# Kernel optimization log

Hardware: AMD Instinct MI355X
Metric: run time of the kernel (lower is better)

Reference implementation:

```python
import jax, jax.numpy as jnp
import numpy as np
import math

D_MODEL = 1024
NUM_HEADS = 16
HEAD_DIM = D_MODEL // NUM_HEADS
WINDOW = 5  # positions j with i - W//2 <= j <= i + W//2 are visible


def setup_inputs() -> dict:
    key = jax.random.key(0)
    ks = jax.random.split(key, 9)
    B, S = 2, 2048
    x = jax.random.normal(ks[0], (B, S, D_MODEL), dtype=jnp.float32)
    # Xavier-uniform linear weights [out, in] (torch convention), zero biases
    lim = math.sqrt(6.0 / (D_MODEL + D_MODEL))
    def w(k):
        return jax.random.uniform(k, (D_MODEL, D_MODEL), dtype=jnp.float32, minval=-lim, maxval=lim)
    return {
        'x': x,
        'Wq': w(ks[1]), 'bq': jnp.zeros((D_MODEL,), jnp.float32),
        'Wk': w(ks[2]), 'bk': jnp.zeros((D_MODEL,), jnp.float32),
        'Wv': w(ks[3]), 'bv': jnp.zeros((D_MODEL,), jnp.float32),
        'Wo': w(ks[4]), 'bo': jnp.zeros((D_MODEL,), jnp.float32),
    }


def reference(x, Wq, bq, Wk, bk, Wv, bv, Wo, bo):
    B, S, D = x.shape
    H, hd = NUM_HEADS, HEAD_DIM
    half = WINDOW // 2

    def proj(W, b):
        # torch Linear: y = x @ W.T + b ; split heads -> [B, H, S, hd]
        return (jnp.einsum('bsd,ed->bse', x, W) + b).reshape(B, S, H, hd).transpose(0, 2, 1, 3)

    q = proj(Wq, bq)
    k = proj(Wk, bk)
    v = proj(Wv, bv)

    scores = jnp.einsum('bhqd,bhkd->bhqk', q, k) / jnp.sqrt(jnp.asarray(hd, x.dtype))
    i = jnp.arange(S)[:, None]
    j = jnp.arange(S)[None, :]
    band = (j >= i - half) & (j <= i + half)  # [S, S] local window mask
    scores = jnp.where(band, scores, jnp.asarray(-1e9, x.dtype))
    attn = jax.nn.softmax(scores, axis=-1)  # dropout is identity in eval mode
    out = jnp.einsum('bhqk,bhkd->bhqd', attn, v)
    out = out.transpose(0, 2, 1, 3).reshape(B, S, D)
    return jnp.einsum('bsd,ed->bse', out, Wo) + bo
```

## Files before the change

kernel.cpp:

```cpp
#include <hip/hip_runtime.h>
#include <hip/hip_bf16.h>

typedef __bf16 bf16_t;
typedef __bf16 bf16x4 __attribute__((ext_vector_type(4)));
typedef __bf16 bf16x8 __attribute__((ext_vector_type(8)));
typedef float f32x4 __attribute__((ext_vector_type(4)));

#define S_LEN 2048
#define DMODEL 1024
#define NHEADS 16
#define HDIM 64
#define BROWS 4096
#define QKVN 3072

__device__ __forceinline__ void async16(const void* g, void* l) {
  __builtin_amdgcn_global_load_lds(
      (const __attribute__((address_space(1))) void*)g,
      (__attribute__((address_space(3))) void*)l, 16, 0, 0);
}

__global__ __launch_bounds__(256) void cvt_all_kernel(
    const float* __restrict__ x, const float* __restrict__ Wq,
    const float* __restrict__ Wk, const float* __restrict__ Wv,
    const float* __restrict__ Wo, bf16_t* __restrict__ dst) {
  const int i = blockIdx.x * 256 + threadIdx.x;
  constexpr int XN4 = (BROWS * DMODEL) / 4;
  constexpr int WN4 = (DMODEL * DMODEL) / 4;
  const float* src;
  size_t off;
  if (i < XN4) {
    src = x;
    off = (size_t)i;
  } else {
    const int wi = i - XN4;
    const int w = wi >> 18;
    off = (size_t)(wi & (WN4 - 1));
    src = (w == 0) ? Wq : (w == 1) ? Wk : (w == 2) ? Wv : Wo;
  }
  const float4 v = *(const float4*)(src + off * 4);
  bf16x4 o;
  o[0] = (bf16_t)v.x;
  o[1] = (bf16_t)v.y;
  o[2] = (bf16_t)v.z;
  o[3] = (bf16_t)v.w;
  *(bf16x4*)(dst + (size_t)i * 4) = o;
}

#define BARR __builtin_amdgcn_s_barrier()
#define LGKM0 asm volatile("s_waitcnt lgkmcnt(0)" ::: "memory")
#define VMC10 asm volatile("s_waitcnt vmcnt(10)" ::: "memory")
#define VMC0 asm volatile("s_waitcnt vmcnt(0)" ::: "memory")

__global__ __launch_bounds__(256, 2) void gemm_qkv_kernel(
    const bf16_t* __restrict__ A, const bf16_t* __restrict__ W,
    const float* __restrict__ bq, const float* __restrict__ bk,
    const float* __restrict__ bv, bf16_t* __restrict__ C) {
  constexpr int Kd = 1024;
  __shared__ char lds[81920];
  char* ldsA = lds;
  char* ldsB = lds + 32768;

  const int m0 = blockIdx.x * 128;
  const int n0 = blockIdx.y * 192;

  const int tid = threadIdx.x;
  const int lane = tid & 63;
  const int wid = tid >> 6;
  const int wr = wid >> 1;
  const int wc = wid & 1;
  const int fr = lane & 15;
  const int l16 = lane >> 4;

  f32x4 acc[4][6] = {};
  bf16x8 aS[4][2], bB[6][2];

  auto stageA = [&](int buf, int kt) {
#pragma unroll
    for (int l = 0; l < 4; ++l) {
      const int idx = l * 256 + tid;
      const int r = idx >> 3;
      const int slot = idx & 7;
      async16((const char*)(A + (size_t)(m0 + r) * Kd + kt * 64 +
                            ((slot ^ (r & 7)) << 3)),
              ldsA + buf * 16384 + r * 128 + slot * 16);
    }
  };
  auto stageB = [&](int buf, int kt) {
#pragma unroll
    for (int l = 0; l < 6; ++l) {
      const int idx = l * 256 + tid;
      const int r = idx >> 3;
      const int slot = idx & 7;
      async16((const char*)(W + (size_t)(n0 + r) * Kd + kt * 64 +
                            ((slot ^ (r & 7)) << 3)),
              ldsB + buf * 24576 + r * 128 + slot * 16);
    }
  };

  auto rdA = [&](int buf, int row, int ks) -> bf16x8 {
    return *(const bf16x8*)(ldsA + buf * 16384 + row * 128 +
                            ((((ks << 2) + l16) ^ (row & 7)) << 4));
  };
  auto rdB = [&](int buf, int row, int ks) -> bf16x8 {
    return *(const bf16x8*)(ldsB + buf * 24576 + row * 128 +
                            ((((ks << 2) + l16) ^ (row & 7)) << 4));
  };

  stageA(0, 0);
  stageB(0, 0);
  stageA(1, 1);
  stageB(1, 1);
  VMC10;
  BARR;

#pragma unroll 1
  for (int t = 0; t < 16; ++t) {
    const int buf = t & 1;
#pragma unroll
    for (int m_ = 0; m_ < 4; ++m_)
#pragma unroll
      for (int ks_ = 0; ks_ < 2; ++ks_)
        aS[m_][ks_] = rdA(buf, wr * 64 + m_ * 16 + fr, ks_);
#pragma unroll
    for (int n_ = 0; n_ < 6; ++n_)
#pragma unroll
      for (int ks_ = 0; ks_ < 2; ++ks_)
        bB[n_][ks_] = rdB(buf, wc * 96 + n_ * 16 + fr, ks_);
    LGKM0;
    BARR;
    if (t + 2 < 16) {
      stageA(buf, t + 2);
      stageB(buf, t + 2);
    }
    __builtin_amdgcn_s_setprio(1);
#pragma unroll
    for (int m_ = 0; m_ < 4; ++m_)
#pragma unroll
      for (int n_ = 0; n_ < 6; ++n_)
#pragma unroll
        for (int ks_ = 0; ks_ < 2; ++ks_)
          acc[m_][n_] = __builtin_amdgcn_mfma_f32_16x16x32_bf16(
              aS[m_][ks_], bB[n_][ks_], acc[m_][n_], 0, 0, 0);
    __builtin_amdgcn_s_setprio(0);
    if (t < 15) {
      if (t + 2 < 16) {
        VMC10;
      } else {
        VMC0;
      }
      BARR;
    }
  }

  const int cr = l16 * 4;
#pragma unroll
  for (int nf = 0; nf < 6; ++nf) {
    const int col = n0 + wc * 96 + nf * 16 + fr;
    const int mat = col >> 10;
    const float* bp = (mat == 0) ? bq : (mat == 1) ? bk : bv;
    const float bval = bp[col & 1023];
#pragma unroll
    for (int mf = 0; mf < 4; ++mf) {
      const int row = m0 + wr * 64 + mf * 16 + cr;
#pragma unroll
      for (int r = 0; r < 4; ++r)
        C[(size_t)(row + r) * QKVN + col] = (bf16_t)(acc[mf][nf][r] + bval);
    }
  }
}

__global__ __launch_bounds__(512) void gemm_o_kernel(
    const bf16_t* __restrict__ Adat, const bf16_t* __restrict__ W,
    const float* __restrict__ bias, float* __restrict__ out) {
  constexpr int Kd = 1024, Nd = 1024, BK = 32, NT = Kd / BK;
  __shared__ bf16_t ldsA[2][128 * BK];
  __shared__ bf16_t ldsB[2][128 * BK];

  const int m0 = blockIdx.x * 128;
  const int n0 = blockIdx.y * 128;

  const int tid = threadIdx.x;
  const int lane = tid & 63;
  const int wid = tid >> 6;
  const int wr = wid >> 2;
  const int wc = wid & 3;
  const int fr = lane & 15;
  const int ko = (lane >> 4) * 8;

  f32x4 acc[4][2] = {};

  auto stage = [&](int buf, int t) {
    const int k0 = t * BK;
    const int row = tid >> 2;
    const int kb = (tid & 3) * 16;
    async16((const char*)(Adat + (size_t)(m0 + row) * Kd + k0) + kb,
            (char*)ldsA[buf] + row * 64 + kb);
    async16((const char*)(W + (size_t)(n0 + row) * Kd + k0) + kb,
            (char*)ldsB[buf] + row * 64 + kb);
  };

  auto compute = [&](int buf) {
    bf16x8 af[4], bf[2];
#pragma unroll
    for (int i = 0; i < 4; ++i)
      af[i] = *(const bf16x8*)(ldsA[buf] + (wr * 64 + i * 16 + fr) * BK + ko);
#pragma unroll
    for (int j = 0; j < 2; ++j)
      bf[j] = *(const bf16x8*)(ldsB[buf] + (wc * 32 + j * 16 + fr) * BK + ko);
#pragma unroll
    for (int i = 0; i < 4; ++i)
#pragma unroll
      for (int j = 0; j < 2; ++j)
        acc[i][j] = __builtin_amdgcn_mfma_f32_16x16x32_bf16(af[i], bf[j],
                                                            acc[i][j], 0, 0, 0);
  };

  stage(0, 0);
  __syncthreads();
#pragma unroll 1
  for (int t = 0; t < NT; ++t) {
    if (t + 1 < NT) stage((t + 1) & 1, t + 1);
    compute(t & 1);
    __syncthreads();
  }

  const int cr = (lane >> 4) * 4;
#pragma unroll
  for (int j = 0; j < 2; ++j) {
    const int col = n0 + wc * 32 + j * 16 + fr;
    const float bval = bias[col];
#pragma unroll
    for (int i = 0; i < 4; ++i) {
#pragma unroll
      for (int r = 0; r < 4; ++r) {
        const int row = m0 + wr * 64 + i * 16 + cr + r;
        out[(size_t)row * Nd + col] = acc[i][j][r] + bval;
      }
    }
  }
}

#define CHUNK 256
#define TROWS 260

__global__ __launch_bounds__(256) void attn_kernel(
    const bf16_t* __restrict__ QKV, bf16_t* __restrict__ ctx) {
  __shared__ bf16_t ldsK[TROWS * HDIM];
  __shared__ bf16_t ldsV[TROWS * HDIM];

  const int tid = threadIdx.x;
  const int blk = blockIdx.x;
  const int chunk = blk & 7;
  const int bh = blk >> 3;
  const int h = bh & (NHEADS - 1);
  const int b = bh >> 4;
  const int s0 = chunk * CHUNK;

  const bf16_t* Kb = QKV + (size_t)b * S_LEN * QKVN + DMODEL + h * HDIM;
  const bf16_t* Vb = QKV + (size_t)b * S_LEN * QKVN + 2 * DMODEL + h * HDIM;

#pragma unroll
  for (int j = 0; j < 9; ++j) {
    const int i = j * 256 + tid;
    if (i < TROWS * 8) {
      const int tr = i >> 3;
      const int slot = i & 7;
      const int c = slot ^ (tr & 7);
      int gs = s0 - 2 + tr;
      gs = (gs < 0) ? 0 : (gs >= S_LEN ? S_LEN - 1 : gs);
      async16((const char*)(Kb + (size_t)gs * QKVN) + c * 16,
              (char*)ldsK + i * 16);
      async16((const char*)(Vb + (size_t)gs * QKVN) + c * 16,
              (char*)ldsV + i * 16);
    }
  }

  const int s = s0 + tid;
  const bf16_t* Qrow = QKV + ((size_t)(b * S_LEN) + s) * QKVN + h * HDIM;
  bf16x8 q8[8];
#pragma unroll
  for (int c = 0; c < 8; ++c) q8[c] = *(const bf16x8*)(Qrow + c * 8);
  float qf[64];
#pragma unroll
  for (int c = 0; c < 8; ++c)
#pragma unroll
    for (int e = 0; e < 8; ++e) qf[c * 8 + e] = (float)q8[c][e];

  __syncthreads();

  float sc[5];
#pragma unroll
  for (int jj = 0; jj < 5; ++jj) {
    const int tr = tid + jj;
    float d = 0.f;
#pragma unroll
    for (int c = 0; c < 8; ++c) {
      const bf16x8 k8 = *(const bf16x8*)(ldsK + tr * HDIM + (c ^ (tr & 7)) * 8);
#pragma unroll
      for (int e = 0; e < 8; ++e) d += qf[c * 8 + e] * (float)k8[e];
    }
    const int j = s - 2 + jj;
    sc[jj] = (j < 0 || j >= S_LEN) ? -1e30f : d * 0.125f;
  }

  float m = sc[0];
#pragma unroll
  for (int jj = 1; jj < 5; ++jj) m = fmaxf(m, sc[jj]);
  float p[5], l = 0.f;
#pragma unroll
  for (int jj = 0; jj < 5; ++jj) {
    p[jj] = __expf(sc[jj] - m);
    l += p[jj];
  }
  const float inv = 1.0f / l;
#pragma unroll
  for (int jj = 0; jj < 5; ++jj) p[jj] *= inv;

  float o[64];
#pragma unroll
  for (int e = 0; e < 64; ++e) o[e] = 0.f;
#pragma unroll
  for (int jj = 0; jj < 5; ++jj) {
    const int tr = tid + jj;
    const float pj = p[jj];
#pragma unroll
    for (int c = 0; c < 8; ++c) {
      const bf16x8 v8 = *(const bf16x8*)(ldsV + tr * HDIM + (c ^ (tr & 7)) * 8);
#pragma unroll
      for (int e = 0; e < 8; ++e) o[c * 8 + e] += pj * (float)v8[e];
    }
  }

  bf16_t* Crow = (bf16_t*)ctx + ((size_t)(b * S_LEN) + s) * DMODEL + h * HDIM;
#pragma unroll
  for (int c = 0; c < 8; ++c) {
    bf16x8 ov;
#pragma unroll
    for (int e = 0; e < 8; ++e) ov[e] = (bf16_t)o[c * 8 + e];
    *(bf16x8*)(Crow + c * 8) = ov;
  }
}

extern "C" void kernel_launch(void* const* d_in, const int* in_sizes, int n_in,
                              void* d_out, int out_size, void* d_ws,
                              size_t ws_size, hipStream_t stream) {
  const float* x = (const float*)d_in[0];
  const float* Wq = (const float*)d_in[1];
  const float* bq = (const float*)d_in[2];
  const float* Wk = (const float*)d_in[3];
  const float* bk = (const float*)d_in[4];
  const float* Wv = (const float*)d_in[5];
  const float* bv = (const float*)d_in[6];
  const float* Wo = (const float*)d_in[7];
  const float* bo = (const float*)d_in[8];
  float* out = (float*)d_out;

  const size_t mat = (size_t)BROWS * DMODEL;
  const size_t wmat = (size_t)DMODEL * DMODEL;
  bf16_t* xb = (bf16_t*)d_ws;
  bf16_t* Wqkv = xb + mat;
  bf16_t* Wob = Wqkv + 3 * wmat;
  bf16_t* QKV = Wob + wmat;
  bf16_t* ctx = QKV + 3 * mat;

  cvt_all_kernel<<<8192, 256, 0, stream>>>(x, Wq, Wk, Wv, Wo, xb);
  gemm_qkv_kernel<<<dim3(32, 16), 256, 0, stream>>>(xb, Wqkv, bq, bk, bv,
                                                    QKV);
  attn_kernel<<<256, 256, 0, stream>>>(QKV, ctx);
  gemm_o_kernel<<<dim3(32, 8), 512, 0, stream>>>(ctx, Wob, bo, out);
}
```

Baseline: 73.39 us.

## Rewrite output projection GEMM with 64x128 tiles, BK=64, swizzled LDS and prefetching

The output projection GEMM moves from 128x128 tiles with 512 threads and BK=32 to 64x128 tiles with 128 threads, BK=64, and 512 blocks. It uses an XOR-swizzled LDS layout to avoid bank conflicts and a two-stage async prefetch with explicit vmcnt waits. MFMA sections run at raised wave priority. The aim is more blocks to fill the CUs, fewer barriers per K step, and less LDS conflict cost, at the price of more register use per wave.

After: 68.10 us, median of 2. 1.08x faster.

```diff
diff --git a/kernel.cpp b/kernel.cpp
--- a/kernel.cpp
+++ b/kernel.cpp
@@ -49,6 +49,7 @@
 #define BARR __builtin_amdgcn_s_barrier()
 #define LGKM0 asm volatile("s_waitcnt lgkmcnt(0)" ::: "memory")
 #define VMC10 asm volatile("s_waitcnt vmcnt(10)" ::: "memory")
+#define VMC12 asm volatile("s_waitcnt vmcnt(12)" ::: "memory")
 #define VMC0 asm volatile("s_waitcnt vmcnt(0)" ::: "memory")
 
 __global__ __launch_bounds__(256, 2) void gemm_qkv_kernel(
@@ -169,73 +170,115 @@
   }
 }
 
-__global__ __launch_bounds__(512) void gemm_o_kernel(
-    const bf16_t* __restrict__ Adat, const bf16_t* __restrict__ W,
+__global__ __launch_bounds__(128) void gemm_o_kernel(
+    const bf16_t* __restrict__ A, const bf16_t* __restrict__ W,
     const float* __restrict__ bias, float* __restrict__ out) {
-  constexpr int Kd = 1024, Nd = 1024, BK = 32, NT = Kd / BK;
-  __shared__ bf16_t ldsA[2][128 * BK];
-  __shared__ bf16_t ldsB[2][128 * BK];
-
-  const int m0 = blockIdx.x * 128;
+  constexpr int Kd = 1024, Nd = 1024;
+  __shared__ char lds[49152];
+  char* ldsA = lds;
+  char* ldsB = lds + 16384;
+
+  const int m0 = blockIdx.x * 64;
   const int n0 = blockIdx.y * 128;
 
   const int tid = threadIdx.x;
   const int lane = tid & 63;
   const int wid = tid >> 6;
-  const int wr = wid >> 2;
-  const int wc = wid & 3;
   const int fr = lane & 15;
-  const int ko = (lane >> 4) * 8;
-
-  f32x4 acc[4][2] = {};
-
-  auto stage = [&](int buf, int t) {
-    const int k0 = t * BK;
-    const int row = tid >> 2;
-    const int kb = (tid & 3) * 16;
-    async16((const char*)(Adat + (size_t)(m0 + row) * Kd + k0) + kb,
-            (char*)ldsA[buf] + row * 64 + kb);
-    async16((const char*)(W + (size_t)(n0 + row) * Kd + k0) + kb,
-            (char*)ldsB[buf] + row * 64 + kb);
-  };
-
-  auto compute = [&](int buf) {
-    bf16x8 af[4], bf[2];
-#pragma unroll
-    for (int i = 0; i < 4; ++i)
-      af[i] = *(const bf16x8*)(ldsA[buf] + (wr * 64 + i * 16 + fr) * BK + ko);
-#pragma unroll
-    for (int j = 0; j < 2; ++j)
-      bf[j] = *(const bf16x8*)(ldsB[buf] + (wc * 32 + j * 16 + fr) * BK + ko);
-#pragma unroll
-    for (int i = 0; i < 4; ++i)
-#pragma unroll
-      for (int j = 0; j < 2; ++j)
-        acc[i][j] = __builtin_amdgcn_mfma_f32_16x16x32_bf16(af[i], bf[j],
-                                                            acc[i][j], 0, 0, 0);
-  };
-
-  stage(0, 0);
-  __syncthreads();
+  const int l16 = lane >> 4;
+
+  f32x4 acc[4][4] = {};
+  bf16x8 aS[4][2], bB[4][2];
+
+  auto stageA = [&](int buf, int kt) {
+#pragma unroll
+    for (int l = 0; l < 4; ++l) {
+      const int idx = l * 128 + tid;
+      const int r = idx >> 3;
+      const int slot = idx & 7;
+      async16((const char*)(A + (size_t)(m0 + r) * Kd + kt * 64 +
+                            ((slot ^ (r & 7)) << 3)),
+              ldsA + buf * 8192 + r * 128 + slot * 16);
+    }
+  };
+  auto stageB = [&](int buf, int kt) {
+#pragma unroll
+    for (int l = 0; l < 8; ++l) {
+      const int idx = l * 128 + tid;
+      const int r = idx >> 3;
+      const int slot = idx & 7;
+      async16((const char*)(W + (size_t)(n0 + r) * Kd + kt * 64 +
+                            ((slot ^ (r & 7)) << 3)),
+              ldsB + buf * 16384 + r * 128 + slot * 16);
+    }
+  };
+
+  auto rdA = [&](int buf, int row, int ks) -> bf16x8 {
+    return *(const bf16x8*)(ldsA + buf * 8192 + row * 128 +
+                            ((((ks << 2) + l16) ^ (row & 7)) << 4));
+  };
+  auto rdB = [&](int buf, int row, int ks) -> bf16x8 {
+    return *(const bf16x8*)(ldsB + buf * 16384 + row * 128 +
+                            ((((ks << 2) + l16) ^ (row & 7)) << 4));
+  };
+
+  stageA(0, 0);
+  stageB(0, 0);
+  stageA(1, 1);
+  stageB(1, 1);
+  VMC12;
+  BARR;
+
 #pragma unroll 1
-  for (int t = 0; t < NT; ++t) {
-    if (t + 1 < NT) stage((t + 1) & 1, t + 1);
-    compute(t & 1);
-    __syncthreads();
-  }
-
-  const int cr = (lane >> 4) * 4;
-#pragma unroll
-  for (int j = 0; j < 2; ++j) {
-    const int col = n0 + wc * 32 + j * 16 + fr;
+  for (int t = 0; t < 16; ++t) {
+    const int buf = t & 1;
+#pragma unroll
+    for (int m_ = 0; m_ < 4; ++m_)
+#pragma unroll
+      for (int ks_ = 0; ks_ < 2; ++ks_)
+        aS[m_][ks_] = rdA(buf, m_ * 16 + fr, ks_);
+#pragma unroll
+    for (int n_ = 0; n_ < 4; ++n_)
+#pragma unroll
+      for (int ks_ = 0; ks_ < 2; ++ks_)
+        bB[n_][ks_] = rdB(buf, wid * 64 + n_ * 16 + fr, ks_);
+    LGKM0;
+    BARR;
+    if (t + 2 < 16) {
+      stageA(buf, t + 2);
+      stageB(buf, t + 2);
+    }
+    __builtin_amdgcn_s_setprio(1);
+#pragma unroll
+    for (int m_ = 0; m_ < 4; ++m_)
+#pragma unroll
+      for (int n_ = 0; n_ < 4; ++n_)
+#pragma unroll
+        for (int ks_ = 0; ks_ < 2; ++ks_)
+          acc[m_][n_] = __builtin_amdgcn_mfma_f32_16x16x32_bf16(
+              aS[m_][ks_], bB[n_][ks_], acc[m_][n_], 0, 0, 0);
+    __builtin_amdgcn_s_setprio(0);
+    if (t < 15) {
+      if (t + 2 < 16) {
+        VMC12;
+      } else {
+        VMC0;
+      }
+      BARR;
+    }
+  }
+
+  const int cr = l16 * 4;
+#pragma unroll
+  for (int nf = 0; nf < 4; ++nf) {
+    const int col = n0 + wid * 64 + nf * 16 + fr;
     const float bval = bias[col];
 #pragma unroll
-    for (int i = 0; i < 4; ++i) {
-#pragma unroll
-      for (int r = 0; r < 4; ++r) {
-        const int row = m0 + wr * 64 + i * 16 + cr + r;
-        out[(size_t)row * Nd + col] = acc[i][j][r] + bval;
-      }
+    for (int mf = 0; mf < 4; ++mf) {
+      const int row = m0 + mf * 16 + cr;
+#pragma unroll
+      for (int r = 0; r < 4; ++r)
+        out[(size_t)(row + r) * Nd + col] = acc[mf][nf][r] + bval;
     }
   }
 }
@@ -367,5 +410,5 @@
   gemm_qkv_kernel<<<dim3(32, 16), 256, 0, stream>>>(xb, Wqkv, bq, bk, bv,
                                                     QKV);
   attn_kernel<<<256, 256, 0, stream>>>(QKV, ctx);
-  gemm_o_kernel<<<dim3(32, 8), 512, 0, stream>>>(ctx, Wob, bo, out);
-}
+  gemm_o_kernel<<<dim3(64, 8), 128, 0, stream>>>(ctx, Wob, bo, out);
+}
```
